# Performance work log

Hardware: AMD Instinct MI355X
Metric: run time of the kernel (lower is better)

The kernel has to match this reference:

```python
import jax, jax.numpy as jnp
import numpy as np

N_NODES = 50000


def setup_inputs() -> dict:
    key = jax.random.key(0)
    k1, k2, k3, k4 = jax.random.split(key, 4)
    N, E, F_IN, F_OUT = N_NODES, 1600000, 512, 128
    x = jax.random.normal(k1, (N, F_IN), dtype=jnp.float32)
    edge_index = jax.random.randint(k2, (2, E), 0, N, dtype=jnp.int64)
    edge_weight = jax.random.uniform(k3, (E,), dtype=jnp.float32)
    # glorot init for weight, zeros bias (as in the original layer)
    limit = np.sqrt(6.0 / (F_IN + F_OUT)).astype(np.float32)
    weight = jax.random.uniform(k4, (F_IN, F_OUT), dtype=jnp.float32,
                                minval=-limit, maxval=limit)
    bias = jnp.zeros((F_OUT,), dtype=jnp.float32)
    return {"x": x, "edge_index": edge_index, "edge_weight": edge_weight,
            "weight": weight, "bias": bias}


def reference(x, edge_index, edge_weight, weight, bias):
    # dropout rate is 0 in this config -> identity
    h = x @ weight                                # [N, F_out] dense transform
    src, dst = edge_index[0], edge_index[1]
    # support @ h : sparse adjacency aggregation (SpMM) via gather + segment_sum
    msgs = h[src] * edge_weight[:, None]          # [E, F_out]
    agg = jax.ops.segment_sum(msgs, dst, num_segments=N_NODES)  # [N, F_out]
    return jax.nn.relu(agg + bias)
```

## Files before the change

### kernel.cpp

```cpp
#include <hip/hip_runtime.h>

#define F_IN  512
#define F_OUT 128
#define FBIN  32
#define EPB   4096
#define C2MAX 1600
#define CAPF  2048

typedef __attribute__((ext_vector_type(8))) short  short8;
typedef __attribute__((ext_vector_type(4))) float  floatx4;

__device__ __forceinline__ unsigned short f2bf(float f) {
    unsigned u = __float_as_uint(f);
    return (unsigned short)((u + 0x7FFF + ((u >> 16) & 1)) >> 16);
}
__device__ __forceinline__ float bf2f(unsigned b) {
    return __uint_as_float(b << 16);
}

__global__ __launch_bounds__(256) void prep(
    const float* __restrict__ w, unsigned short* __restrict__ wt,
    int* __restrict__ cursor, int C2)
{
    const int tid = threadIdx.x;
    if ((int)blockIdx.x < 128) {
        int g0 = blockIdx.x * 512 + tid;
        #pragma unroll
        for (int r = 0; r < 2; ++r) {
            int gid = g0 + r * 256;
            int n = gid >> 9, k = gid & 511;
            wt[gid] = f2bf(w[(size_t)k * F_OUT + n]);
        }
    } else {
        int c = ((int)blockIdx.x - 128) * 256 + tid;
        if (c < C2) cursor[c] = 0;
    }
}

__global__ __launch_bounds__(256, 2) void fill_gemm(
    const int* __restrict__ ei, const float* __restrict__ ew,
    int* __restrict__ cursor, uint2* __restrict__ ent, int E, int C2, int FB,
    const float* __restrict__ x, const unsigned short* __restrict__ wt,
    unsigned short* __restrict__ h, int N)
{
    __shared__ __align__(16) char smem[(64 * 68 + 128 * 68) * 2];
    const int tid = threadIdx.x;

    if ((int)blockIdx.x < FB) {
        int* lh    = (int*)smem;
        int* lbase = (int*)smem + C2MAX;
        for (int c = tid; c < C2; c += 256) lh[c] = 0;
        __syncthreads();

        const int base = blockIdx.x * EPB;
        unsigned       mykey[EPB / 256];
        unsigned char  mydl[EPB / 256];
        short          mybin[EPB / 256];
        unsigned short myrank[EPB / 256];

        #pragma unroll
        for (int j = 0; j < EPB / 256; ++j) {
            int e = base + j * 256 + tid;
            mybin[j] = -1;
            if (e < E) {
                int   src = ei[e];
                int   dst = ei[E + e];
                float w   = ew[e];
                int bin = dst >> 5;
                mykey[j]  = (unsigned)src | ((unsigned)f2bf(w) << 16);
                mydl[j]   = (unsigned char)(dst & (FBIN - 1));
                mybin[j]  = (short)bin;
                myrank[j] = (unsigned short)atomicAdd(&lh[bin], 1);
            }
        }
        __syncthreads();
        for (int c = tid; c < C2; c += 256)
            if (lh[c] > 0) lbase[c] = atomicAdd(&cursor[c], lh[c]);
        __syncthreads();
        #pragma unroll
        for (int j = 0; j < EPB / 256; ++j) {
            if (mybin[j] >= 0) {
                int o = lbase[mybin[j]] + myrank[j];
                if (o < CAPF)
                    ent[(size_t)(int)mybin[j] * CAPF + o] = make_uint2(mykey[j], mydl[j]);
            }
        }
        return;
    }

    unsigned short* sa = (unsigned short*)smem;
    unsigned short* sb = sa + 64 * 68;

    const int wave = tid >> 6, lane = tid & 63;
    const int wm   = wave >> 1, wn = wave & 1;
    const int g    = lane >> 4, l16 = lane & 15;
    const int m0   = ((int)blockIdx.x - FB) * 64;

    const int arow = tid >> 2, aq = tid & 3;
    const int brow = tid >> 1, bh = tid & 1;

    floatx4 acc[2][4];
    #pragma unroll
    for (int rt = 0; rt < 2; ++rt)
        #pragma unroll
        for (int nt = 0; nt < 4; ++nt) acc[rt][nt] = (floatx4)(0.f);

    const bool  avalid = (m0 + arow) < N;
    const float* xp = x + (size_t)(m0 + arow) * F_IN + aq * 16;
    const unsigned short* bp = wt + brow * F_IN + bh * 32;

    float4 ax[4];
    uint4  bv[4];
    #pragma unroll
    for (int i = 0; i < 4; ++i) ax[i] = make_float4(0.f, 0.f, 0.f, 0.f);
    if (avalid) {
        #pragma unroll
        for (int i = 0; i < 4; ++i) ax[i] = ((const float4*)xp)[i];
    }
    #pragma unroll
    for (int i = 0; i < 4; ++i) bv[i] = ((const uint4*)bp)[i];

    for (int s = 0; s < 8; ++s) {
        __syncthreads();
        #pragma unroll
        for (int i = 0; i < 4; ++i) {
            ushort4 t;
            t.x = f2bf(ax[i].x); t.y = f2bf(ax[i].y);
            t.z = f2bf(ax[i].z); t.w = f2bf(ax[i].w);
            *(ushort4*)&sa[arow * 68 + aq * 16 + i * 4] = t;
        }
        #pragma unroll
        for (int i = 0; i < 4; ++i) {
            *(uint2*)&sb[brow * 68 + bh * 32 + i * 8]     = make_uint2(bv[i].x, bv[i].y);
            *(uint2*)&sb[brow * 68 + bh * 32 + i * 8 + 4] = make_uint2(bv[i].z, bv[i].w);
        }
        if (s < 7) {
            int k0n = (s + 1) * 64;
            if (avalid) {
                #pragma unroll
                for (int i = 0; i < 4; ++i) ax[i] = ((const float4*)(xp + k0n))[i];
            }
            #pragma unroll
            for (int i = 0; i < 4; ++i) bv[i] = ((const uint4*)(bp + k0n))[i];
        }
        __syncthreads();

        #pragma unroll
        for (int kc = 0; kc < 2; ++kc) {
            union { ushort4 u[2]; short8 v; } af[2];
            #pragma unroll
            for (int rt = 0; rt < 2; ++rt) {
                int abase = (wm * 32 + rt * 16 + l16) * 68 + kc * 32 + g * 8;
                af[rt].u[0] = *(ushort4*)&sa[abase];
                af[rt].u[1] = *(ushort4*)&sa[abase + 4];
            }
            #pragma unroll
            for (int nt = 0; nt < 4; ++nt) {
                union { ushort4 u[2]; short8 v; } bf;
                int bbase = (wn * 64 + nt * 16 + l16) * 68 + kc * 32 + g * 8;
                bf.u[0] = *(ushort4*)&sb[bbase];
                bf.u[1] = *(ushort4*)&sb[bbase + 4];
                #pragma unroll
                for (int rt = 0; rt < 2; ++rt)
                    acc[rt][nt] = __builtin_amdgcn_mfma_f32_16x16x32_bf16(
                        af[rt].v, bf.v, acc[rt][nt], 0, 0, 0);
            }
        }
    }

    #pragma unroll
    for (int rt = 0; rt < 2; ++rt) {
        #pragma unroll
        for (int nt = 0; nt < 4; ++nt) {
            #pragma unroll
            for (int r = 0; r < 4; ++r) {
                int row = m0 + wm * 32 + rt * 16 + g * 4 + r;
                int col = wn * 64 + nt * 16 + l16;
                if (row < N) h[(size_t)row * F_OUT + col] = f2bf(acc[rt][nt][r]);
            }
        }
    }
}

__global__ __launch_bounds__(256) void fine_agg(
    const unsigned short* __restrict__ h, const uint2* __restrict__ ent,
    const int* __restrict__ cursor, const float* __restrict__ bias,
    float* __restrict__ out, int N, int E,
    const int* __restrict__ ei, const float* __restrict__ ew)
{
    __shared__ unsigned ssort[CAPF];
    __shared__ int lh[FBIN], lcur[FBIN];
    __shared__ int sso[FBIN + 1];

    const int b    = blockIdx.x;
    const int tid  = threadIdx.x;
    const int wave = tid >> 6;
    const int lane = tid & 63;
    const int half = lane >> 5;
    const int q    = lane & 31;
    const float4 bv = *(const float4*)&bias[q * 4];
    const int raw  = cursor[b];
    const int cnt  = raw < CAPF ? raw : CAPF;
    const uint2* slab = ent + (size_t)b * CAPF;

    if (tid < FBIN) lh[tid] = 0;
    __syncthreads();

    for (int i = tid; i < cnt; i += 256)
        atomicAdd(&lh[(int)slab[i].y], 1);
    __syncthreads();

    if (wave == 0 && lane < FBIN) {
        int v = lh[lane];
        int orig = v;
        #pragma unroll
        for (int off = 1; off < FBIN; off <<= 1) {
            int t = __shfl_up(v, off);
            if (lane >= off) v += t;
        }
        sso[lane]  = v - orig;
        lcur[lane] = v - orig;
        if (lane == FBIN - 1) sso[FBIN] = v;
    }
    __syncthreads();

    if (raw <= CAPF) {
        for (int i = tid; i < cnt; i += 256) {
            uint2 e = slab[i];
            int r = atomicAdd(&lcur[(int)e.y], 1);
            ssort[r] = e.x;
        }
        __syncthreads();

        #pragma unroll 1
        for (int t = 0; t < 8; ++t) {
            int nd   = wave * 8 + t;
            int node = b * FBIN + nd;
            int s = sso[nd], e2 = sso[nd + 1];
            float4 acc = make_float4(0.f, 0.f, 0.f, 0.f);
            for (int i = s; i < e2; i += 8) {
                #pragma unroll
                for (int j = 0; j < 4; ++j) {
                    int idx = i + j * 2 + half;
                    unsigned bk = 0;
                    if (idx < e2) bk = ssort[idx];
                    float wgt = bf2f(bk >> 16);
                    uint2 hv = *(const uint2*)&h[(size_t)(bk & 0xFFFF) * F_OUT + q * 4];
                    acc.x += bf2f(hv.x & 0xFFFF) * wgt;
                    acc.y += bf2f(hv.x >> 16)    * wgt;
                    acc.z += bf2f(hv.y & 0xFFFF) * wgt;
                    acc.w += bf2f(hv.y >> 16)    * wgt;
                }
            }
            acc.x += __shfl_xor(acc.x, 32);
            acc.y += __shfl_xor(acc.y, 32);
            acc.z += __shfl_xor(acc.z, 32);
            acc.w += __shfl_xor(acc.w, 32);
            if (half == 0 && node < N) {
                float4 o;
                o.x = fmaxf(acc.x + bv.x, 0.f);
                o.y = fmaxf(acc.y + bv.y, 0.f);
                o.z = fmaxf(acc.z + bv.z, 0.f);
                o.w = fmaxf(acc.w + bv.w, 0.f);
                *(float4*)&out[(size_t)node * F_OUT + q * 4] = o;
            }
        }
    } else {
        #pragma unroll 1
        for (int t = 0; t < 8; ++t) {
            int nd   = wave * 8 + t;
            int node = b * FBIN + nd;
            float4 acc = make_float4(0.f, 0.f, 0.f, 0.f);
            for (int e = half; e < E; e += 2) {
                if (ei[E + e] == node) {
                    float wgt = ew[e];
                    uint2 hv = *(const uint2*)&h[(size_t)ei[e] * F_OUT + q * 4];
                    acc.x += bf2f(hv.x & 0xFFFF) * wgt;
                    acc.y += bf2f(hv.x >> 16)    * wgt;
                    acc.z += bf2f(hv.y & 0xFFFF) * wgt;
                    acc.w += bf2f(hv.y >> 16)    * wgt;
                }
            }
            acc.x += __shfl_xor(acc.x, 32);
            acc.y += __shfl_xor(acc.y, 32);
            acc.z += __shfl_xor(acc.z, 32);
            acc.w += __shfl_xor(acc.w, 32);
            if (half == 0 && node < N) {
                float4 o;
                o.x = fmaxf(acc.x + bv.x, 0.f);
                o.y = fmaxf(acc.y + bv.y, 0.f);
                o.z = fmaxf(acc.z + bv.z, 0.f);
                o.w = fmaxf(acc.w + bv.w, 0.f);
                *(float4*)&out[(size_t)node * F_OUT + q * 4] = o;
            }
        }
    }
}

static inline size_t align256(size_t x) { return (x + 255) & ~(size_t)255; }

extern "C" void kernel_launch(void* const* d_in, const int* in_sizes, int n_in,
                              void* d_out, int out_size, void* d_ws, size_t ws_size,
                              hipStream_t stream)
{
    const float* x    = (const float*)d_in[0];
    const int*   ei   = (const int*)  d_in[1];
    const float* ew   = (const float*)d_in[2];
    const float* w    = (const float*)d_in[3];
    const float* bias = (const float*)d_in[4];
    float*       out  = (float*)d_out;

    const int N  = in_sizes[0] / F_IN;
    const int E  = in_sizes[2];
    const int C2 = (N + FBIN - 1) / FBIN;

    char*  ws = (char*)d_ws;
    size_t off = 0;
    unsigned short* h      = (unsigned short*)(ws + off); off += align256((size_t)N * F_OUT * 2);
    unsigned short* wt     = (unsigned short*)(ws + off); off += align256((size_t)F_OUT * F_IN * 2);
    int*            cursor = (int*)(ws + off);            off += align256((size_t)C2 * 4);
    uint2*          ent    = (uint2*)(ws + off);          off += align256((size_t)C2 * CAPF * 8);

    const int FB = (E + EPB - 1) / EPB;
    const int GB = (N + 63) / 64;
    const int ZB = (C2 + 255) / 256;

    prep<<<128 + ZB, 256, 0, stream>>>(w, wt, cursor, C2);
    fill_gemm<<<FB + GB, 256, 0, stream>>>(ei, ew, cursor, ent, E, C2, FB,
                                           x, wt, h, N);
    fine_agg<<<C2, 256, 0, stream>>>(h, ent, cursor, bias, out, N, E, ei, ew);
}
```

Baseline: 252.8 us.

## Fuse three kernels into one persistent kernel with grid-wide barriers

Merges the prep, fill/GEMM and aggregation kernels into a single persistent kernel of 1024 blocks that loops over work units and separates the phases with atomic-counter grid barriers. This removes two kernel launch boundaries and the tail idle between phases. In exchange it adds a memset launch for the barrier counters and spin-wait overhead. It also relies on all 1024 blocks being co-resident, which needs 4 blocks per CU and risks deadlock if that occupancy is not reached. The grid-stride loops also change the load balance compared with one block per work unit.

```diff
diff --git a/kernel.cpp b/kernel.cpp
--- a/kernel.cpp
+++ b/kernel.cpp
@@ -6,6 +6,7 @@
 #define EPB   4096
 #define C2MAX 1600
 #define CAPF  2048
+#define GRID  1024
 
 typedef __attribute__((ext_vector_type(8))) short  short8;
 typedef __attribute__((ext_vector_type(4))) float  floatx4;
@@ -18,281 +19,297 @@
     return __uint_as_float(b << 16);
 }
 
-__global__ __launch_bounds__(256) void prep(
-    const float* __restrict__ w, unsigned short* __restrict__ wt,
-    int* __restrict__ cursor, int C2)
-{
-    const int tid = threadIdx.x;
-    if ((int)blockIdx.x < 128) {
-        int g0 = blockIdx.x * 512 + tid;
-        #pragma unroll
-        for (int r = 0; r < 2; ++r) {
-            int gid = g0 + r * 256;
-            int n = gid >> 9, k = gid & 511;
-            wt[gid] = f2bf(w[(size_t)k * F_OUT + n]);
-        }
-    } else {
-        int c = ((int)blockIdx.x - 128) * 256 + tid;
-        if (c < C2) cursor[c] = 0;
+__device__ __forceinline__ void grid_barrier(int* cnt, int G) {
+    __threadfence();
+    __syncthreads();
+    if (threadIdx.x == 0) {
+        atomicAdd(cnt, 1);
+        while (atomicAdd(cnt, 0) < G) __builtin_amdgcn_s_sleep(8);
     }
-}
-
-__global__ __launch_bounds__(256, 2) void fill_gemm(
+    __syncthreads();
+    __threadfence();
+}
+
+__global__ __launch_bounds__(256, 4) void fused(
     const int* __restrict__ ei, const float* __restrict__ ew,
-    int* __restrict__ cursor, uint2* __restrict__ ent, int E, int C2, int FB,
-    const float* __restrict__ x, const unsigned short* __restrict__ wt,
-    unsigned short* __restrict__ h, int N)
+    const float* __restrict__ x, const float* __restrict__ w,
+    const float* __restrict__ bias, float* __restrict__ out,
+    unsigned short* __restrict__ h, unsigned short* __restrict__ wt,
+    int* __restrict__ cursor, uint2* __restrict__ ent, int* __restrict__ bar,
+    int N, int E, int C2, int FB, int GB)
 {
     __shared__ __align__(16) char smem[(64 * 68 + 128 * 68) * 2];
     const int tid = threadIdx.x;
-
-    if ((int)blockIdx.x < FB) {
-        int* lh    = (int*)smem;
-        int* lbase = (int*)smem + C2MAX;
-        for (int c = tid; c < C2; c += 256) lh[c] = 0;
-        __syncthreads();
-
-        const int base = blockIdx.x * EPB;
-        unsigned       mykey[EPB / 256];
-        unsigned char  mydl[EPB / 256];
-        short          mybin[EPB / 256];
-        unsigned short myrank[EPB / 256];
-
-        #pragma unroll
-        for (int j = 0; j < EPB / 256; ++j) {
-            int e = base + j * 256 + tid;
-            mybin[j] = -1;
-            if (e < E) {
-                int   src = ei[e];
-                int   dst = ei[E + e];
-                float w   = ew[e];
-                int bin = dst >> 5;
-                mykey[j]  = (unsigned)src | ((unsigned)f2bf(w) << 16);
-                mydl[j]   = (unsigned char)(dst & (FBIN - 1));
-                mybin[j]  = (short)bin;
-                myrank[j] = (unsigned short)atomicAdd(&lh[bin], 1);
-            }
-        }
-        __syncthreads();
-        for (int c = tid; c < C2; c += 256)
-            if (lh[c] > 0) lbase[c] = atomicAdd(&cursor[c], lh[c]);
-        __syncthreads();
-        #pragma unroll
-        for (int j = 0; j < EPB / 256; ++j) {
-            if (mybin[j] >= 0) {
-                int o = lbase[mybin[j]] + myrank[j];
-                if (o < CAPF)
-                    ent[(size_t)(int)mybin[j] * CAPF + o] = make_uint2(mykey[j], mydl[j]);
-            }
-        }
-        return;
-    }
-
-    unsigned short* sa = (unsigned short*)smem;
-    unsigned short* sb = sa + 64 * 68;
-
-    const int wave = tid >> 6, lane = tid & 63;
-    const int wm   = wave >> 1, wn = wave & 1;
-    const int g    = lane >> 4, l16 = lane & 15;
-    const int m0   = ((int)blockIdx.x - FB) * 64;
-
-    const int arow = tid >> 2, aq = tid & 3;
-    const int brow = tid >> 1, bh = tid & 1;
-
-    floatx4 acc[2][4];
-    #pragma unroll
-    for (int rt = 0; rt < 2; ++rt)
-        #pragma unroll
-        for (int nt = 0; nt < 4; ++nt) acc[rt][nt] = (floatx4)(0.f);
-
-    const bool  avalid = (m0 + arow) < N;
-    const float* xp = x + (size_t)(m0 + arow) * F_IN + aq * 16;
-    const unsigned short* bp = wt + brow * F_IN + bh * 32;
-
-    float4 ax[4];
-    uint4  bv[4];
-    #pragma unroll
-    for (int i = 0; i < 4; ++i) ax[i] = make_float4(0.f, 0.f, 0.f, 0.f);
-    if (avalid) {
-        #pragma unroll
-        for (int i = 0; i < 4; ++i) ax[i] = ((const float4*)xp)[i];
-    }
-    #pragma unroll
-    for (int i = 0; i < 4; ++i) bv[i] = ((const uint4*)bp)[i];
-
-    for (int s = 0; s < 8; ++s) {
-        __syncthreads();
-        #pragma unroll
-        for (int i = 0; i < 4; ++i) {
-            ushort4 t;
-            t.x = f2bf(ax[i].x); t.y = f2bf(ax[i].y);
-            t.z = f2bf(ax[i].z); t.w = f2bf(ax[i].w);
-            *(ushort4*)&sa[arow * 68 + aq * 16 + i * 4] = t;
-        }
-        #pragma unroll
-        for (int i = 0; i < 4; ++i) {
-            *(uint2*)&sb[brow * 68 + bh * 32 + i * 8]     = make_uint2(bv[i].x, bv[i].y);
-            *(uint2*)&sb[brow * 68 + bh * 32 + i * 8 + 4] = make_uint2(bv[i].z, bv[i].w);
-        }
-        if (s < 7) {
-            int k0n = (s + 1) * 64;
-            if (avalid) {
-                #pragma unroll
-                for (int i = 0; i < 4; ++i) ax[i] = ((const float4*)(xp + k0n))[i];
-            }
-            #pragma unroll
-            for (int i = 0; i < 4; ++i) bv[i] = ((const uint4*)(bp + k0n))[i];
-        }
-        __syncthreads();
-
-        #pragma unroll
-        for (int kc = 0; kc < 2; ++kc) {
-            union { ushort4 u[2]; short8 v; } af[2];
-            #pragma unroll
-            for (int rt = 0; rt < 2; ++rt) {
-                int abase = (wm * 32 + rt * 16 + l16) * 68 + kc * 32 + g * 8;
-                af[rt].u[0] = *(ushort4*)&sa[abase];
-                af[rt].u[1] = *(ushort4*)&sa[abase + 4];
-            }
-            #pragma unroll
-            for (int nt = 0; nt < 4; ++nt) {
-                union { ushort4 u[2]; short8 v; } bf;
-                int bbase = (wn * 64 + nt * 16 + l16) * 68 + kc * 32 + g * 8;
-                bf.u[0] = *(ushort4*)&sb[bbase];
-                bf.u[1] = *(ushort4*)&sb[bbase + 4];
-                #pragma unroll
-                for (int rt = 0; rt < 2; ++rt)
-                    acc[rt][nt] = __builtin_amdgcn_mfma_f32_16x16x32_bf16(
-                        af[rt].v, bf.v, acc[rt][nt], 0, 0, 0);
+    const int G   = (int)gridDim.x;
+
+    {
+        const int ZB = (C2 + 255) >> 8;
+        for (int u = (int)blockIdx.x; u < 128 + ZB; u += G) {
+            if (u < 128) {
+                int g0 = u * 512 + tid;
+                #pragma unroll
+                for (int r = 0; r < 2; ++r) {
+                    int gid = g0 + r * 256;
+                    int n = gid >> 9, k = gid & 511;
+                    wt[gid] = f2bf(w[(size_t)k * F_OUT + n]);
+                }
+            } else {
+                int c = (u - 128) * 256 + tid;
+                if (c < C2) cursor[c] = 0;
             }
         }
     }
-
-    #pragma unroll
-    for (int rt = 0; rt < 2; ++rt) {
-        #pragma unroll
-        for (int nt = 0; nt < 4; ++nt) {
-            #pragma unroll
-            for (int r = 0; r < 4; ++r) {
-                int row = m0 + wm * 32 + rt * 16 + g * 4 + r;
-                int col = wn * 64 + nt * 16 + l16;
-                if (row < N) h[(size_t)row * F_OUT + col] = f2bf(acc[rt][nt][r]);
-            }
+    grid_barrier(&bar[0], G);
+
+    for (int u = (int)blockIdx.x; u < FB + GB; u += G) {
+        if (u < FB) {
+            int* lh    = (int*)smem;
+            int* lbase = (int*)smem + C2MAX;
+            for (int c = tid; c < C2; c += 256) lh[c] = 0;
+            __syncthreads();
+
+            const int base = u * EPB;
+            unsigned       mykey[EPB / 256];
+            unsigned char  mydl[EPB / 256];
+            short          mybin[EPB / 256];
+            unsigned short myrank[EPB / 256];
+
+            #pragma unroll
+            for (int j = 0; j < EPB / 256; ++j) {
+                int e = base + j * 256 + tid;
+                mybin[j] = -1;
+                if (e < E) {
+                    int   src = ei[e];
+                    int   dst = ei[E + e];
+                    float wv  = ew[e];
+                    int bin = dst >> 5;
+                    mykey[j]  = (unsigned)src | ((unsigned)f2bf(wv) << 16);
+                    mydl[j]   = (unsigned char)(dst & (FBIN - 1));
+                    mybin[j]  = (short)bin;
+                    myrank[j] = (unsigned short)atomicAdd(&lh[bin], 1);
+                }
+            }
+            __syncthreads();
+            for (int c = tid; c < C2; c += 256)
+                if (lh[c] > 0) lbase[c] = atomicAdd(&cursor[c], lh[c]);
+            __syncthreads();
+            #pragma unroll
+            for (int j = 0; j < EPB / 256; ++j) {
+                if (mybin[j] >= 0) {
+                    int o = lbase[mybin[j]] + myrank[j];
+                    if (o < CAPF)
+                        ent[(size_t)(int)mybin[j] * CAPF + o] = make_uint2(mykey[j], mydl[j]);
+                }
+            }
+            __syncthreads();
+        } else {
+            unsigned short* sa = (unsigned short*)smem;
+            unsigned short* sb = sa + 64 * 68;
+
+            const int wave = tid >> 6, lane = tid & 63;
+            const int wm   = wave >> 1, wn = wave & 1;
+            const int g    = lane >> 4, l16 = lane & 15;
+            const int m0   = (u - FB) * 64;
+
+            const int arow = tid >> 2, aq = tid & 3;
+            const int brow = tid >> 1, bh = tid & 1;
+
+            floatx4 acc[2][4];
+            #pragma unroll
+            for (int rt = 0; rt < 2; ++rt)
+                #pragma unroll
+                for (int nt = 0; nt < 4; ++nt) acc[rt][nt] = (floatx4)(0.f);
+
+            const bool  avalid = (m0 + arow) < N;
+            const float* xp = x + (size_t)(m0 + arow) * F_IN + aq * 16;
+            const unsigned short* bp = wt + brow * F_IN + bh * 32;
+
+            float4 ax[4];
+            uint4  bv[4];
+            #pragma unroll
+            for (int i = 0; i < 4; ++i) ax[i] = make_float4(0.f, 0.f, 0.f, 0.f);
+            if (avalid) {
+                #pragma unroll
+                for (int i = 0; i < 4; ++i) ax[i] = ((const float4*)xp)[i];
+            }
+            #pragma unroll
+            for (int i = 0; i < 4; ++i) bv[i] = ((const uint4*)bp)[i];
+
+            for (int s = 0; s < 8; ++s) {
+                __syncthreads();
+                #pragma unroll
+                for (int i = 0; i < 4; ++i) {
+                    ushort4 t;
+                    t.x = f2bf(ax[i].x); t.y = f2bf(ax[i].y);
+                    t.z = f2bf(ax[i].z); t.w = f2bf(ax[i].w);
+                    *(ushort4*)&sa[arow * 68 + aq * 16 + i * 4] = t;
+                }
+                #pragma unroll
+                for (int i = 0; i < 4; ++i) {
+                    *(uint2*)&sb[brow * 68 + bh * 32 + i * 8]     = make_uint2(bv[i].x, bv[i].y);
+                    *(uint2*)&sb[brow * 68 + bh * 32 + i * 8 + 4] = make_uint2(bv[i].z, bv[i].w);
+                }
+                if (s < 7) {
+                    int k0n = (s + 1) * 64;
+                    if (avalid) {
+                        #pragma unroll
+                        for (int i = 0; i < 4; ++i) ax[i] = ((const float4*)(xp + k0n))[i];
+                    }
+                    #pragma unroll
+                    for (int i = 0; i < 4; ++i) bv[i] = ((const uint4*)(bp + k0n))[i];
+                }
+                __syncthreads();
+
+                #pragma unroll
+                for (int kc = 0; kc < 2; ++kc) {
+                    union { ushort4 uu[2]; short8 v; } af[2];
+                    #pragma unroll
+                    for (int rt = 0; rt < 2; ++rt) {
+                        int abase = (wm * 32 + rt * 16 + l16) * 68 + kc * 32 + g * 8;
+                        af[rt].uu[0] = *(ushort4*)&sa[abase];
+                        af[rt].uu[1] = *(ushort4*)&sa[abase + 4];
+                    }
+                    #pragma unroll
+                    for (int nt = 0; nt < 4; ++nt) {
+                        union { ushort4 uu[2]; short8 v; } bf;
+                        int bbase = (wn * 64 + nt * 16 + l16) * 68 + kc * 32 + g * 8;
+                        bf.uu[0] = *(ushort4*)&sb[bbase];
+                        bf.uu[1] = *(ushort4*)&sb[bbase + 4];
+                        #pragma unroll
+                        for (int rt = 0; rt < 2; ++rt)
+                            acc[rt][nt] = __builtin_amdgcn_mfma_f32_16x16x32_bf16(
+                                af[rt].v, bf.v, acc[rt][nt], 0, 0, 0);
+                    }
+                }
+            }
+
+            #pragma unroll
+            for (int rt = 0; rt < 2; ++rt) {
+                #pragma unroll
+                for (int nt = 0; nt < 4; ++nt) {
+                    #pragma unroll
+                    for (int r = 0; r < 4; ++r) {
+                        int row = m0 + wm * 32 + rt * 16 + g * 4 + r;
+                        int col = wn * 64 + nt * 16 + l16;
+                        if (row < N) h[(size_t)row * F_OUT + col] = f2bf(acc[rt][nt][r]);
+                    }
+                }
+            }
+            __syncthreads();
         }
     }
-}
-
-__global__ __launch_bounds__(256) void fine_agg(
-    const unsigned short* __restrict__ h, const uint2* __restrict__ ent,
-    const int* __restrict__ cursor, const float* __restrict__ bias,
-    float* __restrict__ out, int N, int E,
-    const int* __restrict__ ei, const float* __restrict__ ew)
-{
-    __shared__ unsigned ssort[CAPF];
-    __shared__ int lh[FBIN], lcur[FBIN];
-    __shared__ int sso[FBIN + 1];
-
-    const int b    = blockIdx.x;
-    const int tid  = threadIdx.x;
-    const int wave = tid >> 6;
-    const int lane = tid & 63;
-    const int half = lane >> 5;
-    const int q    = lane & 31;
-    const float4 bv = *(const float4*)&bias[q * 4];
-    const int raw  = cursor[b];
-    const int cnt  = raw < CAPF ? raw : CAPF;
-    const uint2* slab = ent + (size_t)b * CAPF;
-
-    if (tid < FBIN) lh[tid] = 0;
-    __syncthreads();
-
-    for (int i = tid; i < cnt; i += 256)
-        atomicAdd(&lh[(int)slab[i].y], 1);
-    __syncthreads();
-
-    if (wave == 0 && lane < FBIN) {
-        int v = lh[lane];
-        int orig = v;
-        #pragma unroll
-        for (int off = 1; off < FBIN; off <<= 1) {
-            int t = __shfl_up(v, off);
-            if (lane >= off) v += t;
-        }
-        sso[lane]  = v - orig;
-        lcur[lane] = v - orig;
-        if (lane == FBIN - 1) sso[FBIN] = v;
-    }
-    __syncthreads();
-
-    if (raw <= CAPF) {
-        for (int i = tid; i < cnt; i += 256) {
-            uint2 e = slab[i];
-            int r = atomicAdd(&lcur[(int)e.y], 1);
-            ssort[r] = e.x;
-        }
-        __syncthreads();
-
-        #pragma unroll 1
-        for (int t = 0; t < 8; ++t) {
-            int nd   = wave * 8 + t;
-            int node = b * FBIN + nd;
-            int s = sso[nd], e2 = sso[nd + 1];
-            float4 acc = make_float4(0.f, 0.f, 0.f, 0.f);
-            for (int i = s; i < e2; i += 8) {
-                #pragma unroll
-                for (int j = 0; j < 4; ++j) {
-                    int idx = i + j * 2 + half;
-                    unsigned bk = 0;
-                    if (idx < e2) bk = ssort[idx];
-                    float wgt = bf2f(bk >> 16);
-                    uint2 hv = *(const uint2*)&h[(size_t)(bk & 0xFFFF) * F_OUT + q * 4];
-                    acc.x += bf2f(hv.x & 0xFFFF) * wgt;
-                    acc.y += bf2f(hv.x >> 16)    * wgt;
-                    acc.z += bf2f(hv.y & 0xFFFF) * wgt;
-                    acc.w += bf2f(hv.y >> 16)    * wgt;
-                }
-            }
-            acc.x += __shfl_xor(acc.x, 32);
-            acc.y += __shfl_xor(acc.y, 32);
-            acc.z += __shfl_xor(acc.z, 32);
-            acc.w += __shfl_xor(acc.w, 32);
-            if (half == 0 && node < N) {
-                float4 o;
-                o.x = fmaxf(acc.x + bv.x, 0.f);
-                o.y = fmaxf(acc.y + bv.y, 0.f);
-                o.z = fmaxf(acc.z + bv.z, 0.f);
-                o.w = fmaxf(acc.w + bv.w, 0.f);
-                *(float4*)&out[(size_t)node * F_OUT + q * 4] = o;
-            }
-        }
-    } else {
-        #pragma unroll 1
-        for (int t = 0; t < 8; ++t) {
-            int nd   = wave * 8 + t;
-            int node = b * FBIN + nd;
-            float4 acc = make_float4(0.f, 0.f, 0.f, 0.f);
-            for (int e = half; e < E; e += 2) {
-                if (ei[E + e] == node) {
-                    float wgt = ew[e];
-                    uint2 hv = *(const uint2*)&h[(size_t)ei[e] * F_OUT + q * 4];
-                    acc.x += bf2f(hv.x & 0xFFFF) * wgt;
-                    acc.y += bf2f(hv.x >> 16)    * wgt;
-                    acc.z += bf2f(hv.y & 0xFFFF) * wgt;
-                    acc.w += bf2f(hv.y >> 16)    * wgt;
-                }
-            }
-            acc.x += __shfl_xor(acc.x, 32);
-            acc.y += __shfl_xor(acc.y, 32);
-            acc.z += __shfl_xor(acc.z, 32);
-            acc.w += __shfl_xor(acc.w, 32);
-            if (half == 0 && node < N) {
-                float4 o;
-                o.x = fmaxf(acc.x + bv.x, 0.f);
-                o.y = fmaxf(acc.y + bv.y, 0.f);
-                o.z = fmaxf(acc.z + bv.z, 0.f);
-                o.w = fmaxf(acc.w + bv.w, 0.f);
-                *(float4*)&out[(size_t)node * F_OUT + q * 4] = o;
-            }
+    grid_barrier(&bar[1], G);
+
+    {
+        unsigned* ssort = (unsigned*)smem;
+        int* lh   = (int*)(smem + CAPF * 4);
+        int* lcur = lh + FBIN;
+        int* sso  = lcur + FBIN;
+
+        const int wave = tid >> 6;
+        const int lane = tid & 63;
+        const int half = lane >> 5;
+        const int q    = lane & 31;
+        const float4 bvb = *(const float4*)&bias[q * 4];
+
+        for (int b = (int)blockIdx.x; b < C2; b += G) {
+            const int raw = cursor[b];
+            const int cnt = raw < CAPF ? raw : CAPF;
+            const uint2* slab = ent + (size_t)b * CAPF;
+
+            if (tid < FBIN) lh[tid] = 0;
+            __syncthreads();
+
+            for (int i = tid; i < cnt; i += 256)
+                atomicAdd(&lh[(int)slab[i].y], 1);
+            __syncthreads();
+
+            if (wave == 0 && lane < FBIN) {
+                int v = lh[lane];
+                int orig = v;
+                #pragma unroll
+                for (int off = 1; off < FBIN; off <<= 1) {
+                    int t = __shfl_up(v, off);
+                    if (lane >= off) v += t;
+                }
+                sso[lane]  = v - orig;
+                lcur[lane] = v - orig;
+                if (lane == FBIN - 1) sso[FBIN] = v;
+            }
+            __syncthreads();
+
+            if (raw <= CAPF) {
+                for (int i = tid; i < cnt; i += 256) {
+                    uint2 e = slab[i];
+                    int r = atomicAdd(&lcur[(int)e.y], 1);
+                    ssort[r] = e.x;
+                }
+                __syncthreads();
+
+                #pragma unroll 1
+                for (int t = 0; t < 8; ++t) {
+                    int nd   = wave * 8 + t;
+                    int node = b * FBIN + nd;
+                    int s = sso[nd], e2 = sso[nd + 1];
+                    float4 acc = make_float4(0.f, 0.f, 0.f, 0.f);
+                    for (int i = s; i < e2; i += 8) {
+                        #pragma unroll
+                        for (int j = 0; j < 4; ++j) {
+                            int idx = i + j * 2 + half;
+                            unsigned bk = 0;
+                            if (idx < e2) bk = ssort[idx];
+                            float wgt = bf2f(bk >> 16);
+                            uint2 hv = *(const uint2*)&h[(size_t)(bk & 0xFFFF) * F_OUT + q * 4];
+                            acc.x += bf2f(hv.x & 0xFFFF) * wgt;
+                            acc.y += bf2f(hv.x >> 16)    * wgt;
+                            acc.z += bf2f(hv.y & 0xFFFF) * wgt;
+                            acc.w += bf2f(hv.y >> 16)    * wgt;
+                        }
+                    }
+                    acc.x += __shfl_xor(acc.x, 32);
+                    acc.y += __shfl_xor(acc.y, 32);
+                    acc.z += __shfl_xor(acc.z, 32);
+                    acc.w += __shfl_xor(acc.w, 32);
+                    if (half == 0 && node < N) {
+                        float4 o;
+                        o.x = fmaxf(acc.x + bvb.x, 0.f);
+                        o.y = fmaxf(acc.y + bvb.y, 0.f);
+                        o.z = fmaxf(acc.z + bvb.z, 0.f);
+                        o.w = fmaxf(acc.w + bvb.w, 0.f);
+                        *(float4*)&out[(size_t)node * F_OUT + q * 4] = o;
+                    }
+                }
+            } else {
+                #pragma unroll 1
+                for (int t = 0; t < 8; ++t) {
+                    int nd   = wave * 8 + t;
+                    int node = b * FBIN + nd;
+                    float4 acc = make_float4(0.f, 0.f, 0.f, 0.f);
+                    for (int e = half; e < E; e += 2) {
+                        if (ei[E + e] == node) {
+                            float wgt = ew[e];
+                            uint2 hv = *(const uint2*)&h[(size_t)ei[e] * F_OUT + q * 4];
+                            acc.x += bf2f(hv.x & 0xFFFF) * wgt;
+                            acc.y += bf2f(hv.x >> 16)    * wgt;
+                            acc.z += bf2f(hv.y & 0xFFFF) * wgt;
+                            acc.w += bf2f(hv.y >> 16)    * wgt;
+                        }
+                    }
+                    acc.x += __shfl_xor(acc.x, 32);
+                    acc.y += __shfl_xor(acc.y, 32);
+                    acc.z += __shfl_xor(acc.z, 32);
+                    acc.w += __shfl_xor(acc.w, 32);
+                    if (half == 0 && node < N) {
+                        float4 o;
+                        o.x = fmaxf(acc.x + bvb.x, 0.f);
+                        o.y = fmaxf(acc.y + bvb.y, 0.f);
+                        o.z = fmaxf(acc.z + bvb.z, 0.f);
+                        o.w = fmaxf(acc.w + bvb.w, 0.f);
+                        *(float4*)&out[(size_t)node * F_OUT + q * 4] = o;
+                    }
+                }
+            }
+            __syncthreads();
         }
     }
 }
@@ -319,14 +336,13 @@
     unsigned short* h      = (unsigned short*)(ws + off); off += align256((size_t)N * F_OUT * 2);
     unsigned short* wt     = (unsigned short*)(ws + off); off += align256((size_t)F_OUT * F_IN * 2);
     int*            cursor = (int*)(ws + off);            off += align256((size_t)C2 * 4);
+    int*            bar    = (int*)(ws + off);            off += align256(2 * sizeof(int));
     uint2*          ent    = (uint2*)(ws + off);          off += align256((size_t)C2 * CAPF * 8);
 
     const int FB = (E + EPB - 1) / EPB;
     const int GB = (N + 63) / 64;
-    const int ZB = (C2 + 255) / 256;
-
-    prep<<<128 + ZB, 256, 0, stream>>>(w, wt, cursor, C2);
-    fill_gemm<<<FB + GB, 256, 0, stream>>>(ei, ew, cursor, ent, E, C2, FB,
-                                           x, wt, h, N);
-    fine_agg<<<C2, 256, 0, stream>>>(h, ent, cursor, bias, out, N, E, ei, ew);
-}
+
+    (void)hipMemsetAsync(bar, 0, 2 * sizeof(int), stream);
+    fused<<<GRID, 256, 0, stream>>>(ei, ew, x, w, bias, out, h, wt, cursor, ent,
+                                    bar, N, E, C2, FB, GB);
+}
```

Result: slower. 873.1 us (+245.4%).
